# Optimization experiments

Hardware: AMD Instinct MI355X
Metric: run time of the kernel (lower is better)

The kernel has to match this reference:

```python
import jax, jax.numpy as jnp
import numpy as np

D = 512          # token_dim * num_heads
TOKEN_DIM = 256
SCALE = TOKEN_DIM ** (-0.5)


def _l2norm(x, axis):
    # torch.nn.functional.normalize: x / max(||x||_2, eps)
    n = jnp.linalg.norm(x, axis=axis, keepdims=True)
    return x / jnp.maximum(n, 1e-12)


def setup_inputs() -> dict:
    key = jax.random.key(0)
    ks = jax.random.split(key, 32)
    B, N, IN = 8, 4096, 512
    s_in = 1.0 / np.sqrt(IN)
    s_d = 1.0 / np.sqrt(D)

    def lin(k, fin, fout, scale):
        kw, kb = jax.random.split(k)
        return (jax.random.uniform(kw, (fin, fout), jnp.float32, -scale, scale),
                jax.random.uniform(kb, (fout,), jnp.float32, -scale, scale))

    wq_I, bq_I = lin(ks[0], IN, D, s_in)
    wk_I, bk_I = lin(ks[1], IN, D, s_in)
    wq_M, bq_M = lin(ks[2], IN, D, s_in)
    wk_M, bk_M = lin(ks[3], IN, D, s_in)
    p1_w, p1_b = lin(ks[4], D, D, s_d)
    p2_w, p2_b = lin(ks[5], D, D, s_d)
    p3_w, p3_b = lin(ks[6], D, D, s_d)
    p4_w, p4_b = lin(ks[7], D, D, s_d)
    f_w, f_b = lin(ks[8], D, TOKEN_DIM, s_d)
    return {
        'x_I': jax.random.normal(ks[9], (B, N, IN), jnp.float32),
        'x_M': jax.random.normal(ks[10], (B, N, IN), jnp.float32),
        'wq_I': wq_I, 'bq_I': bq_I, 'wk_I': wk_I, 'bk_I': bk_I,
        'wq_M': wq_M, 'bq_M': bq_M, 'wk_M': wk_M, 'bk_M': bk_M,
        'wg_I': jax.random.normal(ks[11], (D, 1), jnp.float32),
        'wg_M': jax.random.normal(ks[12], (D, 1), jnp.float32),
        'p1_w': p1_w, 'p1_b': p1_b, 'p2_w': p2_w, 'p2_b': p2_b,
        'p3_w': p3_w, 'p3_b': p3_b, 'p4_w': p4_w, 'p4_b': p4_b,
        'f_w': f_w, 'f_b': f_b,
    }


def reference(x_I, x_M, wq_I, bq_I, wk_I, bk_I, wq_M, bq_M, wk_M, bk_M,
              wg_I, wg_M, p1_w, p1_b, p2_w, p2_b, p3_w, p3_b, p4_w, p4_b,
              f_w, f_b):
    # projections, then L2-normalize along feature dim
    q_I = _l2norm(x_I @ wq_I + bq_I, axis=-1)   # [B, N, D]
    k_I = _l2norm(x_I @ wk_I + bk_I, axis=-1)
    q_M = _l2norm(x_M @ wq_M + bq_M, axis=-1)
    k_M = _l2norm(x_M @ wk_M + bk_M, axis=-1)

    # softmax-free attention weights, L2-normalized over sequence dim
    A_I = _l2norm((q_I @ wg_I) * SCALE, axis=1)  # [B, N, 1]
    A_M = _l2norm((q_M @ wg_M) * SCALE, axis=1)

    # pooled global queries, broadcast back over tokens
    G_I = jnp.sum(A_I * q_I, axis=1, keepdims=True)  # [B, 1, D]
    G_M = jnp.sum(A_M * q_M, axis=1, keepdims=True)

    out = ((G_I * k_I) @ p1_w + p1_b
           + (G_I * k_M) @ p2_w + p2_b
           + (G_M * k_M) @ p3_w + p3_b
           + (G_M * k_I) @ p4_w + p4_b
           + q_I + q_M)                              # [B, N, D]
    return out @ f_w + f_b                           # [B, N, token_dim]
```

## Files before the change

kernel.cpp:

```cpp
#include <hip/hip_runtime.h>

typedef unsigned short u16;
typedef unsigned int   u32;
typedef __bf16 bf16_t;
typedef bf16_t bf16x8 __attribute__((ext_vector_type(8)));
typedef float  f32x4  __attribute__((ext_vector_type(4)));

__device__ __forceinline__ float b2f(u16 u){
  u32 x = ((u32)u) << 16;
  return __builtin_bit_cast(float, x);
}
__device__ __forceinline__ u16 f2b(float f){
  u32 u = __builtin_bit_cast(u32, f);
  u32 r = u + 0x7FFFu + ((u >> 16) & 1u);
  return (u16)(r >> 16);
}

union V8 { uint4 q; u16 u[8]; };

__device__ __forceinline__ void gld16(const u16* gsrc, u16* ldst){
  __builtin_amdgcn_global_load_lds(
      (const __attribute__((address_space(1))) u32*)gsrc,
      (__attribute__((address_space(3))) u32*)ldst, 16, 0, 0);
}

struct CArgs { const float* src[4]; u16* dst[4]; int cnt[4]; };

__global__ __launch_bounds__(256) void convert_k(CArgs c){
  int z = blockIdx.z;
  int i8 = (blockIdx.x * 256 + threadIdx.x) * 8;
  if (i8 >= c.cnt[z]) return;
  const float* s = c.src[z] + i8;
  float4 a = *(const float4*)s;
  float4 b = *(const float4*)(s + 4);
  V8 o;
  o.u[0]=f2b(a.x); o.u[1]=f2b(a.y); o.u[2]=f2b(a.z); o.u[3]=f2b(a.w);
  o.u[4]=f2b(b.x); o.u[5]=f2b(b.y); o.u[6]=f2b(b.z); o.u[7]=f2b(b.w);
  *(uint4*)(c.dst[z] + i8) = o.q;
}

struct TArgs { const float* src[5]; u16* dst[5]; int ncol[5]; };

__global__ __launch_bounds__(256) void transpose_k(TArgs t,
    const float* __restrict__ p1b, const float* __restrict__ p2b,
    const float* __restrict__ p3b, const float* __restrict__ p4b,
    const float* __restrict__ fw, const float* __restrict__ fb,
    float* __restrict__ cb, float* __restrict__ Gun)
{
  __shared__ u16 T[64][65];
  __shared__ float sb[512];
  int z = blockIdx.z;
  int tid = threadIdx.x;
  if (z == 5){
    if (blockIdx.x == 0 && blockIdx.y == 0){
      sb[tid]       = p1b[tid] + p2b[tid] + p3b[tid] + p4b[tid];
      sb[tid + 256] = p1b[tid+256] + p2b[tid+256] + p3b[tid+256] + p4b[tid+256];
      __syncthreads();
      float acc = 0.f;
      for (int j = 0; j < 512; j++) acc += sb[j] * fw[j*256 + tid];
      cb[tid] = acc + fb[tid];
    } else if (blockIdx.x >= 1 && blockIdx.x <= 4){
      int idx = ((blockIdx.x - 1)*8 + blockIdx.y)*256 + tid;
      Gun[idx] = 0.f;
    }
    return;
  }
  int nc = t.ncol[z];
  int j0 = blockIdx.y * 64;
  if (j0 >= nc) return;
  int i0 = blockIdx.x * 64;
  const float* s = t.src[z];
  u16* d = t.dst[z];
  #pragma unroll
  for (int rep = 0; rep < 16; rep++){
    int lin = rep*256 + tid;
    int r = lin >> 6, c = lin & 63;
    T[c][r] = f2b(s[(size_t)(i0 + r) * nc + j0 + c]);
  }
  __syncthreads();
  #pragma unroll
  for (int rep = 0; rep < 16; rep++){
    int lin = rep*256 + tid;
    int r = lin >> 6, c = lin & 63;
    d[(size_t)(j0 + r) * 512 + i0 + c] = T[r][c];
  }
}

__global__ __launch_bounds__(256, 2) void proj_k(
    const float* __restrict__ XI, const float* __restrict__ XM,
    const u16* __restrict__ WTI, const u16* __restrict__ WTM,
    const float* __restrict__ bqI, const float* __restrict__ bkI,
    const float* __restrict__ bqM, const float* __restrict__ bkM,
    const float* __restrict__ wgI, const float* __restrict__ wgM,
    u16* __restrict__ qI, u16* __restrict__ kI,
    u16* __restrict__ qM, u16* __restrict__ kM,
    float* __restrict__ Araw, float* __restrict__ Gun)
{
  const int tid = threadIdx.x, l = tid & 63, w = tid >> 6;
  const int m0 = blockIdx.x * 64;
  const int y  = blockIdx.y, zi = blockIdx.z;
  __shared__ __align__(16) u16 As[2][64*32];
  __shared__ __align__(16) u16 Bs[2][512*32];
  const int lr = l & 15, quad = l >> 4;
  const int srow = l >> 2, scol = (l & 3) * 8;
  const int wn = w * 128;

  const float* X  = zi ? XM : XI;
  const u16* Wbase = (zi ? WTM : WTI) + (size_t)y * 512 * 512;
  const float* bias = y ? (zi ? bkM : bkI) : (zi ? bqM : bqI);
  const float* wg   = zi ? wgM : wgI;
  u16* OUT = y ? (zi ? kM : kI) : (zi ? qM : qI);

  const int arow = w*16 + (l >> 2);
  const int aks  = (l & 3) * 8;
  const float* aptr = X + (size_t)(m0 + arow)*512 + aks;

  f32x4 acc[4][8] = {};

  {
    float4 p0 = *(const float4*)(aptr);
    float4 p1 = *(const float4*)(aptr + 4);
    V8 o;
    o.u[0]=f2b(p0.x); o.u[1]=f2b(p0.y); o.u[2]=f2b(p0.z); o.u[3]=f2b(p0.w);
    o.u[4]=f2b(p1.x); o.u[5]=f2b(p1.y); o.u[6]=f2b(p1.z); o.u[7]=f2b(p1.w);
    *(uint4*)&As[0][arow*32 + aks] = o.q;
    #pragma unroll
    for (int i = 0; i < 8; i++)
      gld16(Wbase + (size_t)(wn + i*16 + srow)*512 + scol, &Bs[0][(w*8 + i)*512]);
  }
  __syncthreads();

  #pragma unroll
  for (int kk = 0; kk < 16; kk++){
    const int k0 = kk * 32;
    const int cur = kk & 1, nxt = cur ^ 1;
    const int kn = k0 + 32;
    float4 p0, p1;
    if (kn < 512){
      #pragma unroll
      for (int i = 0; i < 8; i++)
        gld16(Wbase + (size_t)(wn + i*16 + srow)*512 + kn + scol, &Bs[nxt][(w*8 + i)*512]);
      p0 = *(const float4*)(aptr + kn);
      p1 = *(const float4*)(aptr + kn + 4);
    }
    bf16x8 aF[4], bF[8];
    #pragma unroll
    for (int mt = 0; mt < 4; mt++)
      aF[mt] = *(const bf16x8*)&As[cur][(mt*16 + lr)*32 + quad*8];
    #pragma unroll
    for (int nt = 0; nt < 8; nt++)
      bF[nt] = *(const bf16x8*)&Bs[cur][(wn + nt*16 + lr)*32 + quad*8];
    #pragma unroll
    for (int mt = 0; mt < 4; mt++){
      #pragma unroll
      for (int nt = 0; nt < 8; nt++)
        acc[mt][nt] = __builtin_amdgcn_mfma_f32_16x16x32_bf16(aF[mt], bF[nt], acc[mt][nt], 0, 0, 0);
    }
    if (kn < 512){
      V8 o;
      o.u[0]=f2b(p0.x); o.u[1]=f2b(p0.y); o.u[2]=f2b(p0.z); o.u[3]=f2b(p0.w);
      o.u[4]=f2b(p1.x); o.u[5]=f2b(p1.y); o.u[6]=f2b(p1.z); o.u[7]=f2b(p1.w);
      *(uint4*)&As[nxt][arow*32 + aks] = o.q;
    }
    __syncthreads();
  }

  float wgv[8];
  if (y == 0){
    #pragma unroll
    for (int nt = 0; nt < 8; nt++) wgv[nt] = wg[wn + nt*16 + lr];
  }
  #pragma unroll
  for (int nt = 0; nt < 8; nt++){
    float bcol = bias[wn + nt*16 + lr];
    #pragma unroll
    for (int mt = 0; mt < 4; mt++)
      #pragma unroll
      for (int r = 0; r < 4; r++)
        acc[mt][nt][r] += bcol;
  }
  float ss[4][4], dq[4][4];
  #pragma unroll
  for (int mt = 0; mt < 4; mt++)
    #pragma unroll
    for (int r = 0; r < 4; r++){
      float s = 0.f, d = 0.f;
      #pragma unroll
      for (int nt = 0; nt < 8; nt++){
        float v = acc[mt][nt][r];
        s += v*v;
        if (y == 0) d += v * wgv[nt];
      }
      ss[mt][r] = s; dq[mt][r] = d;
    }
  #pragma unroll
  for (int off = 1; off < 16; off <<= 1){
    #pragma unroll
    for (int mt = 0; mt < 4; mt++)
      #pragma unroll
      for (int r = 0; r < 4; r++){
        ss[mt][r] += __shfl_xor(ss[mt][r], off, 64);
        if (y == 0) dq[mt][r] += __shfl_xor(dq[mt][r], off, 64);
      }
  }
  __syncthreads();
  float* red    = (float*)As;
  float* red2   = red + 256;
  float* rnS    = red2 + 256;
  float* araw_s = rnS + 64;
  if (lr == 0){
    #pragma unroll
    for (int mt = 0; mt < 4; mt++)
      #pragma unroll
      for (int r = 0; r < 4; r++){
        int row = mt*16 + quad*4 + r;
        red[w*64 + row] = ss[mt][r];
        if (y == 0) red2[w*64 + row] = dq[mt][r];
      }
  }
  __syncthreads();
  if (tid < 64){
    float t2 = red[tid] + red[64+tid] + red[128+tid] + red[192+tid];
    float rn = 1.f / fmaxf(sqrtf(t2), 1e-12f);
    rnS[tid] = rn;
    if (y == 0){
      float d = red2[tid] + red2[64+tid] + red2[128+tid] + red2[192+tid];
      float a = d * rn * 0.0625f;
      araw_s[tid] = a;
      Araw[zi*32768 + m0 + tid] = a;
    }
  }
  __syncthreads();
  float part[8] = {};
  #pragma unroll
  for (int mt = 0; mt < 4; mt++){
    f32x4 rn4 = *(const f32x4*)&rnS[mt*16 + quad*4];
    #pragma unroll
    for (int r = 0; r < 4; r++){
      float aw = (y == 0) ? araw_s[mt*16 + quad*4 + r] : 0.f;
      #pragma unroll
      for (int nt = 0; nt < 8; nt++){
        float v = acc[mt][nt][r] * rn4[r];
        OUT[(size_t)(m0 + mt*16 + quad*4 + r)*512 + wn + nt*16 + lr] = f2b(v);
        if (y == 0) part[nt] += aw * v;
      }
    }
  }
  if (y == 0){
    #pragma unroll
    for (int nt = 0; nt < 8; nt++){
      part[nt] += __shfl_xor(part[nt], 16, 64);
      part[nt] += __shfl_xor(part[nt], 32, 64);
    }
    if (quad == 0){
      int bb = blockIdx.x >> 6;
      #pragma unroll
      for (int nt = 0; nt < 8; nt++)
        atomicAdd(&Gun[((size_t)zi*8 + bb)*512 + wn + nt*16 + lr], part[nt]);
    }
  }
}

template<int MODE>
__global__ __launch_bounds__(256) void gemm2_k(
    const u16* __restrict__ A0, const u16* __restrict__ A1,
    const u16* __restrict__ A2, const u16* __restrict__ A3,
    const u16* __restrict__ BT,
    const float* __restrict__ cb,
    u16* __restrict__ Cq, float* __restrict__ Cf)
{
  constexpr int KTOT = (MODE == 2) ? 2048 : 512;
  const int tid = threadIdx.x, l = tid & 63, w = tid >> 6;
  const int m0 = blockIdx.x * 128, n0 = blockIdx.y * 128;
  __shared__ u16 As[2][128*32];
  __shared__ u16 Bs[2][128*32];
  f32x4 acc[4][4] = {};
  const int wm = (w >> 1) * 64, wn = (w & 1) * 64;
  const int lr = l & 15, quad = l >> 4;
  const int srow = l >> 2, scol = (l & 3) * 8;

  const u16* Bbase = BT;
  u16* Cqb = Cq;
  if constexpr (MODE == 2)
    Bbase = BT + (size_t)(m0 >> 12) * 256 * 2048;
  if constexpr (MODE == 1){
    Bbase = BT + (size_t)blockIdx.z * 262144;
    Cqb   = Cq + (size_t)blockIdx.z * 131072;
  }

  #pragma unroll
  for (int i = 0; i < 2; i++){
    int r = w*32 + i*16 + srow;
    gld16(A0    + (size_t)(m0 + r) * 512  + scol, &As[0][(w*2 + i) * 512]);
    gld16(Bbase + (size_t)(n0 + r) * KTOT + scol, &Bs[0][(w*2 + i) * 512]);
  }
  __syncthreads();

  #pragma unroll 2
  for (int k0 = 0; k0 < KTOT; k0 += 32){
    const int cur = (k0 >> 5) & 1, nxt = cur ^ 1;
    const int kn = k0 + 32;
    if (kn < KTOT){
      const u16* Ab; int kloc;
      if constexpr (MODE == 2){
        int which = kn >> 9; kloc = kn & 511;
        Ab = (which == 0) ? A0 : (which == 1) ? A1 : (which == 2) ? A2 : A3;
      } else { Ab = A0; kloc = kn; }
      #pragma unroll
      for (int i = 0; i < 2; i++){
        int r = w*32 + i*16 + srow;
        gld16(Ab    + (size_t)(m0 + r) * 512  + kloc + scol, &As[nxt][(w*2 + i) * 512]);
        gld16(Bbase + (size_t)(n0 + r) * KTOT + kn   + scol, &Bs[nxt][(w*2 + i) * 512]);
      }
    }
    bf16x8 aF[4], bF[4];
    #pragma unroll
    for (int mt = 0; mt < 4; mt++)
      aF[mt] = *(const bf16x8*)&As[cur][(wm + mt*16 + lr)*32 + quad*8];
    #pragma unroll
    for (int nt = 0; nt < 4; nt++)
      bF[nt] = *(const bf16x8*)&Bs[cur][(wn + nt*16 + lr)*32 + quad*8];
    #pragma unroll
    for (int mt = 0; mt < 4; mt++){
      #pragma unroll
      for (int nt = 0; nt < 4; nt++)
        acc[mt][nt] = __builtin_amdgcn_mfma_f32_16x16x32_bf16(aF[mt], bF[nt], acc[mt][nt], 0, 0, 0);
    }
    __syncthreads();
  }

  #pragma unroll
  for (int nt = 0; nt < 4; nt++){
    int col = n0 + wn + nt*16 + lr;
    #pragma unroll
    for (int mt = 0; mt < 4; mt++){
      int row0 = m0 + wm + mt*16 + quad*4;
      #pragma unroll
      for (int r = 0; r < 4; r++){
        int row = row0 + r;
        float v = acc[mt][nt][r];
        if constexpr (MODE == 1){
          Cqb[(size_t)row*512 + col] = f2b(v);
        } else {
          Cf[(size_t)row*256 + col] = v + cb[col];
        }
      }
    }
  }
}

__global__ __launch_bounds__(256) void ranorm_k(const float* __restrict__ Araw,
                                                float* __restrict__ rA){
  int idx = blockIdx.x;
  const float* A = Araw + idx*4096;
  int tid = threadIdx.x, l = tid & 63, w = tid >> 6;
  float ss = 0.f;
  for (int i = tid; i < 4096; i += 256){ float a = A[i]; ss += a*a; }
  #pragma unroll
  for (int off = 32; off > 0; off >>= 1) ss += __shfl_xor(ss, off, 64);
  __shared__ float red[4];
  if (l == 0) red[w] = ss;
  __syncthreads();
  if (tid == 0)
    rA[idx] = 1.f / fmaxf(sqrtf(red[0] + red[1] + red[2] + red[3]), 1e-12f);
}

__global__ __launch_bounds__(256) void weff_k(
    const u16* __restrict__ pfT, const u16* __restrict__ fT,
    const float* __restrict__ Gun, const float* __restrict__ rA,
    u16* __restrict__ WT)
{
  int b = blockIdx.x, o = blockIdx.y, tid = threadIdx.x;
  int k0 = tid * 8;
  V8 out;
  if (k0 < 1024){
    int kk = k0 & 511;
    const u16* pa = pfT + ((k0 < 512) ? 0      : 131072) + o*512 + kk;
    const u16* pb = pfT + ((k0 < 512) ? 393216 : 262144) + o*512 + kk;
    float rI = rA[b], rM = rA[8 + b];
    const float* gI = Gun + b*512 + kk;
    const float* gM = Gun + 4096 + b*512 + kk;
    V8 Pa, Pb; Pa.q = *(const uint4*)pa; Pb.q = *(const uint4*)pb;
    float4 gi0 = *(const float4*)gI, gi1 = *(const float4*)(gI+4);
    float4 gm0 = *(const float4*)gM, gm1 = *(const float4*)(gM+4);
    float gi[8] = {gi0.x,gi0.y,gi0.z,gi0.w,gi1.x,gi1.y,gi1.z,gi1.w};
    float gm[8] = {gm0.x,gm0.y,gm0.z,gm0.w,gm1.x,gm1.y,gm1.z,gm1.w};
    #pragma unroll
    for (int j = 0; j < 8; j++)
      out.u[j] = f2b(rI*gi[j]*b2f(Pa.u[j]) + rM*gm[j]*b2f(Pb.u[j]));
  } else {
    out.q = *(const uint4*)(fT + o*512 + (k0 & 511));
  }
  *(uint4*)(WT + ((size_t)b*256 + o)*2048 + k0) = out.q;
}

extern "C" void kernel_launch(void* const* d_in, const int* in_sizes, int n_in,
                              void* d_out, int out_size, void* d_ws, size_t ws_size,
                              hipStream_t stream)
{
  const float* x_I  = (const float*)d_in[0];
  const float* x_M  = (const float*)d_in[1];
  const float* wq_I = (const float*)d_in[2];
  const float* bq_I = (const float*)d_in[3];
  const float* wk_I = (const float*)d_in[4];
  const float* bk_I = (const float*)d_in[5];
  const float* wq_M = (const float*)d_in[6];
  const float* bq_M = (const float*)d_in[7];
  const float* wk_M = (const float*)d_in[8];
  const float* bk_M = (const float*)d_in[9];
  const float* wg_I = (const float*)d_in[10];
  const float* wg_M = (const float*)d_in[11];
  const float* p1_w = (const float*)d_in[12];
  const float* p1_b = (const float*)d_in[13];
  const float* p2_w = (const float*)d_in[14];
  const float* p2_b = (const float*)d_in[15];
  const float* p3_w = (const float*)d_in[16];
  const float* p3_b = (const float*)d_in[17];
  const float* p4_w = (const float*)d_in[18];
  const float* p4_b = (const float*)d_in[19];
  const float* f_w  = (const float*)d_in[20];
  const float* f_b  = (const float*)d_in[21];

  char* ws = (char*)d_ws;
  u16*  wqkT_I = (u16*)(ws + 0);
  u16*  wqkT_M = (u16*)(ws + 1048576);
  u16*  fT     = (u16*)(ws + 2097152);
  u16*  pcat   = (u16*)(ws + 2359296);
  u16*  pfT    = (u16*)(ws + 4456448);
  u16*  WT     = (u16*)(ws + 5505024);
  float* cb    = (float*)(ws + 13893632);
  float* Araw  = (float*)(ws + 13894656);
  float* rA    = (float*)(ws + 14156800);
  float* Gun   = (float*)(ws + 14157056);
  u16*  qIb    = (u16*)(ws + 14189824);
  u16*  kIb    = (u16*)(ws + 47744256);
  u16*  qMb    = (u16*)(ws + 81298688);
  u16*  kMb    = (u16*)(ws + 114853120);

  CArgs c;
  const float* csrc[4] = {p1_w, p2_w, p3_w, p4_w};
  u16* cdst[4] = {pcat, pcat + 262144, pcat + 524288, pcat + 786432};
  for (int i = 0; i < 4; i++){ c.src[i] = csrc[i]; c.dst[i] = cdst[i]; c.cnt[i] = 262144; }
  convert_k<<<dim3(128,1,4), 256, 0, stream>>>(c);

  TArgs t;
  const float* tsrc[5] = {wq_I, wk_I, wq_M, wk_M, f_w};
  u16* tdst[5] = {wqkT_I, wqkT_I + 262144, wqkT_M, wqkT_M + 262144, fT};
  int tnc[5] = {512, 512, 512, 512, 256};
  for (int i = 0; i < 5; i++){ t.src[i] = tsrc[i]; t.dst[i] = tdst[i]; t.ncol[i] = tnc[i]; }
  transpose_k<<<dim3(8,8,6), 256, 0, stream>>>(t, p1_b, p2_b, p3_b, p4_b, f_w, f_b, cb, Gun);

  gemm2_k<1><<<dim3(2,4,4), 256, 0, stream>>>(fT, nullptr, nullptr, nullptr,
      pcat, nullptr, pfT, nullptr);

  proj_k<<<dim3(512,2,2), 256, 0, stream>>>(x_I, x_M, wqkT_I, wqkT_M,
      bq_I, bk_I, bq_M, bk_M, wg_I, wg_M, qIb, kIb, qMb, kMb, Araw, Gun);

  ranorm_k<<<16, 256, 0, stream>>>(Araw, rA);

  weff_k<<<dim3(8,256), 256, 0, stream>>>(pfT, fT, Gun, rA, WT);

  gemm2_k<2><<<dim3(256,2), 256, 0, stream>>>(kIb, kMb, qIb, qMb,
      WT, cb, nullptr, (float*)d_out);
}
```

Baseline: 392.2 us.

## Make GEMM tiles wave-private to drop block barriers and load A directly

Both the projection kernel and the second GEMM now give each wave its own LDS slices for the tiles it consumes. Each wave waits on its own loads with s_waitcnt instead of a block-wide __syncthreads every k-step. The projection kernel also reads X straight into registers, converting to bf16 per wave, and no longer stages A through shared memory. MFMA priority is raised with s_setprio and gemm2 gets a two-blocks-per-CU launch bound. The cost is duplicated global loads of shared tiles across waves (A in gemm2 loaded twice, X rows per wave) and reliance on manual vmcnt counting being correct.

```diff
diff --git a/kernel.cpp b/kernel.cpp
--- a/kernel.cpp
+++ b/kernel.cpp
@@ -99,70 +99,73 @@
   const int tid = threadIdx.x, l = tid & 63, w = tid >> 6;
   const int m0 = blockIdx.x * 64;
   const int y  = blockIdx.y, zi = blockIdx.z;
-  __shared__ __align__(16) u16 As[2][64*32];
-  __shared__ __align__(16) u16 Bs[2][512*32];
+  __shared__ __align__(16) u16 Bs[2][4][4096];
+  __shared__ float sc[640];
   const int lr = l & 15, quad = l >> 4;
   const int srow = l >> 2, scol = (l & 3) * 8;
   const int wn = w * 128;
 
   const float* X  = zi ? XM : XI;
-  const u16* Wbase = (zi ? WTM : WTI) + (size_t)y * 512 * 512;
+  const u16* Wbase = (zi ? WTM : WTI) + (size_t)y * 512 * 512 + (size_t)wn * 512;
   const float* bias = y ? (zi ? bkM : bkI) : (zi ? bqM : bqI);
   const float* wg   = zi ? wgM : wgI;
   u16* OUT = y ? (zi ? kM : kI) : (zi ? qM : qI);
 
-  const int arow = w*16 + (l >> 2);
-  const int aks  = (l & 3) * 8;
-  const float* aptr = X + (size_t)(m0 + arow)*512 + aks;
+  const float* Xl = X + (size_t)(m0 + lr) * 512 + quad * 8;
 
   f32x4 acc[4][8] = {};
-
-  {
-    float4 p0 = *(const float4*)(aptr);
-    float4 p1 = *(const float4*)(aptr + 4);
-    V8 o;
-    o.u[0]=f2b(p0.x); o.u[1]=f2b(p0.y); o.u[2]=f2b(p0.z); o.u[3]=f2b(p0.w);
-    o.u[4]=f2b(p1.x); o.u[5]=f2b(p1.y); o.u[6]=f2b(p1.z); o.u[7]=f2b(p1.w);
-    *(uint4*)&As[0][arow*32 + aks] = o.q;
-    #pragma unroll
-    for (int i = 0; i < 8; i++)
-      gld16(Wbase + (size_t)(wn + i*16 + srow)*512 + scol, &Bs[0][(w*8 + i)*512]);
-  }
-  __syncthreads();
+  float4 sa0[4], sa1[4];
+
+  #pragma unroll
+  for (int i = 0; i < 8; i++)
+    gld16(Wbase + (size_t)(i*16 + srow)*512 + scol, &Bs[0][w][i*512]);
+  #pragma unroll
+  for (int mt = 0; mt < 4; mt++){
+    const float* p = Xl + (size_t)(mt*16)*512;
+    sa0[mt] = *(const float4*)p;
+    sa1[mt] = *(const float4*)(p + 4);
+  }
 
   #pragma unroll
   for (int kk = 0; kk < 16; kk++){
-    const int k0 = kk * 32;
     const int cur = kk & 1, nxt = cur ^ 1;
-    const int kn = k0 + 32;
-    float4 p0, p1;
+    const int kn = (kk + 1) * 32;
     if (kn < 512){
       #pragma unroll
       for (int i = 0; i < 8; i++)
-        gld16(Wbase + (size_t)(wn + i*16 + srow)*512 + kn + scol, &Bs[nxt][(w*8 + i)*512]);
-      p0 = *(const float4*)(aptr + kn);
-      p1 = *(const float4*)(aptr + kn + 4);
-    }
-    bf16x8 aF[4], bF[8];
-    #pragma unroll
-    for (int mt = 0; mt < 4; mt++)
-      aF[mt] = *(const bf16x8*)&As[cur][(mt*16 + lr)*32 + quad*8];
+        gld16(Wbase + (size_t)(i*16 + srow)*512 + kn + scol, &Bs[nxt][w][i*512]);
+      asm volatile("s_waitcnt vmcnt(8)" ::: "memory");
+    } else {
+      asm volatile("s_waitcnt vmcnt(0)" ::: "memory");
+    }
+    bf16x8 aF[4];
+    #pragma unroll
+    for (int mt = 0; mt < 4; mt++){
+      V8 o;
+      o.u[0]=f2b(sa0[mt].x); o.u[1]=f2b(sa0[mt].y); o.u[2]=f2b(sa0[mt].z); o.u[3]=f2b(sa0[mt].w);
+      o.u[4]=f2b(sa1[mt].x); o.u[5]=f2b(sa1[mt].y); o.u[6]=f2b(sa1[mt].z); o.u[7]=f2b(sa1[mt].w);
+      aF[mt] = __builtin_bit_cast(bf16x8, o.q);
+    }
+    if (kn < 512){
+      #pragma unroll
+      for (int mt = 0; mt < 4; mt++){
+        const float* p = Xl + (size_t)(mt*16)*512 + kn;
+        sa0[mt] = *(const float4*)p;
+        sa1[mt] = *(const float4*)(p + 4);
+      }
+    }
+    bf16x8 bF[8];
     #pragma unroll
     for (int nt = 0; nt < 8; nt++)
-      bF[nt] = *(const bf16x8*)&Bs[cur][(wn + nt*16 + lr)*32 + quad*8];
+      bF[nt] = *(const bf16x8*)&Bs[cur][w][(nt*16 + lr)*32 + quad*8];
+    __builtin_amdgcn_s_setprio(1);
     #pragma unroll
     for (int mt = 0; mt < 4; mt++){
       #pragma unroll
       for (int nt = 0; nt < 8; nt++)
         acc[mt][nt] = __builtin_amdgcn_mfma_f32_16x16x32_bf16(aF[mt], bF[nt], acc[mt][nt], 0, 0, 0);
     }
-    if (kn < 512){
-      V8 o;
-      o.u[0]=f2b(p0.x); o.u[1]=f2b(p0.y); o.u[2]=f2b(p0.z); o.u[3]=f2b(p0.w);
-      o.u[4]=f2b(p1.x); o.u[5]=f2b(p1.y); o.u[6]=f2b(p1.z); o.u[7]=f2b(p1.w);
-      *(uint4*)&As[nxt][arow*32 + aks] = o.q;
-    }
-    __syncthreads();
+    __builtin_amdgcn_s_setprio(0);
   }
 
   float wgv[8];
@@ -203,8 +206,7 @@
         if (y == 0) dq[mt][r] += __shfl_xor(dq[mt][r], off, 64);
       }
   }
-  __syncthreads();
-  float* red    = (float*)As;
+  float* red    = sc;
   float* red2   = red + 256;
   float* rnS    = red2 + 256;
   float* araw_s = rnS + 64;
@@ -262,7 +264,7 @@
 }
 
 template<int MODE>
-__global__ __launch_bounds__(256) void gemm2_k(
+__global__ __launch_bounds__(256, 2) void gemm2_k(
     const u16* __restrict__ A0, const u16* __restrict__ A1,
     const u16* __restrict__ A2, const u16* __restrict__ A3,
     const u16* __restrict__ BT,
@@ -272,8 +274,7 @@
   constexpr int KTOT = (MODE == 2) ? 2048 : 512;
   const int tid = threadIdx.x, l = tid & 63, w = tid >> 6;
   const int m0 = blockIdx.x * 128, n0 = blockIdx.y * 128;
-  __shared__ u16 As[2][128*32];
-  __shared__ u16 Bs[2][128*32];
+  __shared__ __align__(16) u16 S[2][4][2][2048];
   f32x4 acc[4][4] = {};
   const int wm = (w >> 1) * 64, wn = (w & 1) * 64;
   const int lr = l & 15, quad = l >> 4;
@@ -289,12 +290,10 @@
   }
 
   #pragma unroll
-  for (int i = 0; i < 2; i++){
-    int r = w*32 + i*16 + srow;
-    gld16(A0    + (size_t)(m0 + r) * 512  + scol, &As[0][(w*2 + i) * 512]);
-    gld16(Bbase + (size_t)(n0 + r) * KTOT + scol, &Bs[0][(w*2 + i) * 512]);
-  }
-  __syncthreads();
+  for (int i = 0; i < 4; i++){
+    gld16(A0    + (size_t)(m0 + wm + i*16 + srow) * 512  + scol, &S[0][w][0][i*512]);
+    gld16(Bbase + (size_t)(n0 + wn + i*16 + srow) * KTOT + scol, &S[0][w][1][i*512]);
+  }
 
   #pragma unroll 2
   for (int k0 = 0; k0 < KTOT; k0 += 32){
@@ -307,26 +306,29 @@
         Ab = (which == 0) ? A0 : (which == 1) ? A1 : (which == 2) ? A2 : A3;
       } else { Ab = A0; kloc = kn; }
       #pragma unroll
-      for (int i = 0; i < 2; i++){
-        int r = w*32 + i*16 + srow;
-        gld16(Ab    + (size_t)(m0 + r) * 512  + kloc + scol, &As[nxt][(w*2 + i) * 512]);
-        gld16(Bbase + (size_t)(n0 + r) * KTOT + kn   + scol, &Bs[nxt][(w*2 + i) * 512]);
-      }
+      for (int i = 0; i < 4; i++){
+        gld16(Ab    + (size_t)(m0 + wm + i*16 + srow) * 512  + kloc + scol, &S[nxt][w][0][i*512]);
+        gld16(Bbase + (size_t)(n0 + wn + i*16 + srow) * KTOT + kn   + scol, &S[nxt][w][1][i*512]);
+      }
+      asm volatile("s_waitcnt vmcnt(8)" ::: "memory");
+    } else {
+      asm volatile("s_waitcnt vmcnt(0)" ::: "memory");
     }
     bf16x8 aF[4], bF[4];
     #pragma unroll
     for (int mt = 0; mt < 4; mt++)
-      aF[mt] = *(const bf16x8*)&As[cur][(wm + mt*16 + lr)*32 + quad*8];
+      aF[mt] = *(const bf16x8*)&S[cur][w][0][(mt*16 + lr)*32 + quad*8];
     #pragma unroll
     for (int nt = 0; nt < 4; nt++)
-      bF[nt] = *(const bf16x8*)&Bs[cur][(wn + nt*16 + lr)*32 + quad*8];
+      bF[nt] = *(const bf16x8*)&S[cur][w][1][(nt*16 + lr)*32 + quad*8];
+    __builtin_amdgcn_s_setprio(1);
     #pragma unroll
     for (int mt = 0; mt < 4; mt++){
       #pragma unroll
       for (int nt = 0; nt < 4; nt++)
         acc[mt][nt] = __builtin_amdgcn_mfma_f32_16x16x32_bf16(aF[mt], bF[nt], acc[mt][nt], 0, 0, 0);
     }
-    __syncthreads();
+    __builtin_amdgcn_s_setprio(0);
   }
 
   #pragma unroll
```

New measurement: 570.6 us. 1.45x slower.
